# Kernel tuning notes

Measured on AMD Instinct MI355X. Metric: run time of the kernel, lower is better.

The kernel has to match this reference:

```python
import jax, jax.numpy as jnp
import numpy as np

# Module hyperparameters (init_kwargs): dim=128, res=128, idx=0, split_size=8, num_heads=8
B, RES, DIM, NH = 8, 128, 128, 8
HD = DIM // NH               # head_dim = 16
HSP, WSP = RES, 8            # idx=0 -> H_sp=res, W_sp=split_size
N = HSP * WSP                # tokens per window
SCALE = HD ** -0.5
L = RES * RES


def setup_inputs() -> dict:
    key = jax.random.key(0)
    k1, k2, k3 = jax.random.split(key, 3)
    return {
        "qkv": jax.random.normal(k1, (3, B, L, DIM), dtype=jnp.float32),
        "conv_w": jax.random.normal(k2, (DIM, 1, 3, 3), dtype=jnp.float32) * 0.1,
        "conv_b": jax.random.normal(k3, (DIM,), dtype=jnp.float32) * 0.1,
    }


def _im2cswin(x):
    # x: [B, L, C] -> windows as heads: [B*nW, NH, N, HD]
    x = jnp.transpose(x, (0, 2, 1)).reshape(B, DIM, RES, RES)
    x = x.reshape(B, DIM, RES // HSP, HSP, RES // WSP, WSP)
    x = jnp.transpose(x, (0, 2, 4, 3, 5, 1)).reshape(-1, N, DIM)
    x = x.reshape(-1, N, NH, HD)
    return jnp.transpose(x, (0, 2, 1, 3))


def reference(qkv, conv_w, conv_b):
    q, k, v = qkv[0], qkv[1], qkv[2]
    k = _im2cswin(k)                               # [W, NH, N, HD]
    v = _im2cswin(v)                               # [W, NH, N, HD]

    # q -> per-window image blocks [B*nW, C, H_sp, W_sp]
    qi = jnp.transpose(q, (0, 2, 1)).reshape(B, DIM, RES, RES)
    qi = qi.reshape(B, DIM, RES // HSP, HSP, RES // WSP, WSP)
    qi = jnp.transpose(qi, (0, 2, 4, 1, 3, 5)).reshape(-1, DIM, HSP, WSP)

    # depthwise 3x3 conv LePE
    lepe = jax.lax.conv_general_dilated(
        qi, conv_w, window_strides=(1, 1), padding='SAME',
        feature_group_count=DIM,
        dimension_numbers=('NCHW', 'OIHW', 'NCHW'))
    lepe = lepe + conv_b[None, :, None, None]
    lepe = jnp.transpose(lepe.reshape(-1, NH, HD, N), (0, 1, 3, 2))  # [W, NH, N, HD]
    qh = jnp.transpose(qi.reshape(-1, NH, HD, N), (0, 1, 3, 2))      # [W, NH, N, HD]

    # linear attention: softmax over scaled K^T V (d x d)
    att = jnp.einsum('wnid,wnie->wnde', k, v) * SCALE                # [W, NH, HD, HD]
    att = jax.nn.softmax(att, axis=-1)
    x = jnp.einsum('wnid,wnde->wnie', qh, att) + lepe                # [W, NH, N, HD]

    # windows -> image -> [B, L, C]
    x = jnp.transpose(x, (0, 2, 1, 3)).reshape(-1, N, DIM)
    x = x.reshape(B, RES // HSP, RES // WSP, HSP, WSP, DIM)
    x = jnp.transpose(x, (0, 1, 3, 2, 4, 5)).reshape(B, RES, RES, DIM)
    return x.reshape(B, L, DIM)
```

## Files before the change

### kernel.cpp

```cpp
#include <hip/hip_runtime.h>


static constexpr int BB   = 8;
static constexpr int RES  = 128;
static constexpr int DIM  = 128;
static constexpr int WSP  = 8;
static constexpr int L    = RES * RES;
static constexpr float SCALE = 0.25f;

#define GLD_LDS16(g, l)                                                        \
  __builtin_amdgcn_global_load_lds(                                            \
      (const __attribute__((address_space(1))) void*)(const void*)(g),         \
      (__attribute__((address_space(3))) void*)(l), 16, 0, 0)

__global__ __launch_bounds__(256, 2) void fused_lepe(
    const float* __restrict__ Qg, const float* __restrict__ Kg,
    const float* __restrict__ Vg, const float* __restrict__ cw,
    const float* __restrict__ cb, float* __restrict__ outp) {
  __shared__ float smem[16896];
  float* const A_sm = smem + 16384;

  const int b  = blockIdx.x;
  const int w  = b >> 2, g = b & 3;
  const int bi = w >> 4, wb = w & 15;
  const int t  = threadIdx.x;
  const int wave = t >> 6, lane = t & 63;
  const size_t win_base = (size_t)(bi * L + wb * WSP) * DIM;
  const int ch0 = g * 32;

  const int h1 = lane >> 5, dq = (lane >> 3) & 3, ep = lane & 7;
  float a00=0.f,a01=0.f,a10=0.f,a11=0.f,a20=0.f,a21=0.f,a30=0.f,a31=0.f;

  auto stageKV = [&](int tile, int buf) {
    for (int c = wave; c < 32; c += 4) {
      const int mat = c >> 4, rr = c & 15;
      const int r = tile * 16 + rr;
      const float* src = (mat ? Vg : Kg) + win_base +
                         (size_t)r * (RES * DIM) + (lane >> 3) * DIM + ch0 +
                         (lane & 7) * 4;
      float* dst = smem + mat * 8192 + buf * 4096 + rr * 256;
      GLD_LDS16(src, dst);
    }
  };

  stageKV(0, 0);
  __syncthreads();
  for (int tt = 0; tt < 8; ++tt) {
    const int cur = tt & 1;
    if (tt < 7) stageKV(tt + 1, cur ^ 1);
    const float* Kb = smem + cur * 4096;
    const float* Vb = smem + 8192 + cur * 4096;
    const int n0 = wave * 32;
#pragma unroll 4
    for (int n = n0; n < n0 + 32; ++n) {
      const float4 k4 =
          *reinterpret_cast<const float4*>(&Kb[n * 32 + h1 * 16 + dq * 4]);
      const float2 v2 =
          *reinterpret_cast<const float2*>(&Vb[n * 32 + h1 * 16 + ep * 2]);
      a00 += k4.x * v2.x; a01 += k4.x * v2.y;
      a10 += k4.y * v2.x; a11 += k4.y * v2.y;
      a20 += k4.z * v2.x; a21 += k4.z * v2.y;
      a30 += k4.w * v2.x; a31 += k4.w * v2.y;
    }
    __syncthreads();
  }

  auto stageQ = [&](int tile, int buf) {
    const int r0 = tile * 16;
    float* qb = smem + buf * 4608;
    for (int c = wave; c < 18; c += 4) {
      const int r = r0 - 1 + c;
      float* dst = qb + c * 256;
      if ((unsigned)r < 128u) {
        const float* src = Qg + win_base + (size_t)r * (RES * DIM) +
                           (lane >> 3) * DIM + ch0 + (lane & 7) * 4;
        GLD_LDS16(src, dst);
      } else {
        *reinterpret_cast<float4*>(dst + lane * 4) =
            make_float4(0.f, 0.f, 0.f, 0.f);
      }
    }
  };

  stageQ(0, 1);

  {
    float* sc = smem + wave * 512 + lane * 8;
    sc[0]=a00; sc[1]=a01; sc[2]=a10; sc[3]=a11;
    sc[4]=a20; sc[5]=a21; sc[6]=a30; sc[7]=a31;
  }
  __syncthreads();

  {
    const int r  = t >> 3;
    const int e2 = t & 7;
    const int h = r >> 4, d = r & 15;
    const int f = (h * 32 + (d >> 2) * 8 + e2) * 8 + (d & 3) * 2;
    float v0 = smem[f]     + smem[512 + f]     + smem[1024 + f]     + smem[1536 + f];
    float v1 = smem[f + 1] + smem[512 + f + 1] + smem[1024 + f + 1] + smem[1536 + f + 1];
    v0 *= SCALE; v1 *= SCALE;
    float m = fmaxf(v0, v1);
    m = fmaxf(m, __shfl_xor(m, 1));
    m = fmaxf(m, __shfl_xor(m, 2));
    m = fmaxf(m, __shfl_xor(m, 4));
    v0 = __expf(v0 - m); v1 = __expf(v1 - m);
    float ssum = v0 + v1;
    ssum += __shfl_xor(ssum, 1);
    ssum += __shfl_xor(ssum, 2);
    ssum += __shfl_xor(ssum, 4);
    const float rinv = 1.0f / ssum;
    A_sm[r * 16 + e2 * 2 + 0] = v0 * rinv;
    A_sm[r * 16 + e2 * 2 + 1] = v1 * rinv;
  }
  __syncthreads();

  const int cq   = t & 7;
  const int lr   = (t >> 3) & 15;
  const int half = t >> 7;
  const int hg = cq >> 2, e0 = (cq & 3) * 4;
  const int cg = ch0 + cq * 4;

  float4 Acol[16];
#pragma unroll
  for (int d = 0; d < 16; ++d)
    Acol[d] = *reinterpret_cast<const float4*>(&A_sm[(hg * 16 + d) * 16 + e0]);
  float4 wgt[9];
#pragma unroll
  for (int tap = 0; tap < 9; ++tap) {
    wgt[tap].x = cw[(cg + 0) * 9 + tap];
    wgt[tap].y = cw[(cg + 1) * 9 + tap];
    wgt[tap].z = cw[(cg + 2) * 9 + tap];
    wgt[tap].w = cw[(cg + 3) * 9 + tap];
  }
  const float4 bias = *reinterpret_cast<const float4*>(&cb[cg]);

#define ACC(qs, d)                                                             \
  o.x += (qs) * Acol[d].x; o.y += (qs) * Acol[d].y;                            \
  o.z += (qs) * Acol[d].z; o.w += (qs) * Acol[d].w;

  int buf = 1;
  for (int tile = 0; tile < 8; ++tile) {
    if (tile < 7) stageQ(tile + 1, buf ^ 1);
    const float* Qb = smem + buf * 4608;
    const int r0 = tile * 16;
    const int w0 = half * 4;

    float4 cL[3], cC[3], cR[3];
    auto ldcol = [&](int cidx, float4* dstv) {
#pragma unroll
      for (int dy = 0; dy < 3; ++dy)
        dstv[dy] = ((unsigned)cidx < 8u)
                       ? *reinterpret_cast<const float4*>(
                             &Qb[((lr + dy) * 8 + cidx) * 32 + cq * 4])
                       : make_float4(0.f, 0.f, 0.f, 0.f);
    };
    ldcol(w0 - 1, cL);
    ldcol(w0, cC);

#pragma unroll
    for (int k = 0; k < 4; ++k) {
      const int wl = w0 + k;
      ldcol(wl + 1, cR);
      float4 o = bias;
#pragma unroll
      for (int dy = 0; dy < 3; ++dy) {
        const int t0 = dy * 3;
        o.x += cL[dy].x * wgt[t0].x + cC[dy].x * wgt[t0+1].x + cR[dy].x * wgt[t0+2].x;
        o.y += cL[dy].y * wgt[t0].y + cC[dy].y * wgt[t0+1].y + cR[dy].y * wgt[t0+2].y;
        o.z += cL[dy].z * wgt[t0].z + cC[dy].z * wgt[t0+1].z + cR[dy].z * wgt[t0+2].z;
        o.w += cL[dy].w * wgt[t0].w + cC[dy].w * wgt[t0+1].w + cR[dy].w * wgt[t0+2].w;
      }
      const float* qr = &Qb[((lr + 1) * 8 + wl) * 32 + hg * 16];
      const float4 q0 = *reinterpret_cast<const float4*>(qr + 0);
      const float4 q1 = *reinterpret_cast<const float4*>(qr + 4);
      const float4 q2 = *reinterpret_cast<const float4*>(qr + 8);
      const float4 q3 = *reinterpret_cast<const float4*>(qr + 12);
      ACC(q0.x, 0)  ACC(q0.y, 1)  ACC(q0.z, 2)  ACC(q0.w, 3)
      ACC(q1.x, 4)  ACC(q1.y, 5)  ACC(q1.z, 6)  ACC(q1.w, 7)
      ACC(q2.x, 8)  ACC(q2.y, 9)  ACC(q2.z, 10) ACC(q2.w, 11)
      ACC(q3.x, 12) ACC(q3.y, 13) ACC(q3.z, 14) ACC(q3.w, 15)

      float* dst = outp + win_base + (size_t)(r0 + lr) * (RES * DIM) +
                   wl * DIM + cg;
      *reinterpret_cast<float4*>(dst) = o;

#pragma unroll
      for (int dy = 0; dy < 3; ++dy) { cL[dy] = cC[dy]; cC[dy] = cR[dy]; }
    }
    __syncthreads();
    buf ^= 1;
  }
#undef ACC
}

extern "C" void kernel_launch(void* const* d_in, const int* in_sizes, int n_in,
                              void* d_out, int out_size, void* d_ws,
                              size_t ws_size, hipStream_t stream) {
  const float* qkv = (const float*)d_in[0];
  const float* cw  = (const float*)d_in[1];
  const float* cb  = (const float*)d_in[2];
  const float* Qg = qkv;
  const float* Kg = qkv + (size_t)BB * L * DIM;
  const float* Vg = Kg + (size_t)BB * L * DIM;
  float* outp = (float*)d_out;

  fused_lepe<<<512, 256, 0, stream>>>(Qg, Kg, Vg, cw, cb, outp);
}
```

Baseline: 55.29 us.

## Triple-buffer KV staging, retile K^T V accumulation, swizzle Q LDS layout

The K^T V phase now stages 8-row tiles into a three-deep LDS ring, waiting with explicit vmcnt counts and raw barriers so loads run two tiles ahead. Each thread accumulates an 8x4 block from wider float4 reads, and partial sums are reduced across lane groups with shuffles instead of through LDS. The Q staging applies an XOR swizzle on the 16-byte column index, with matching reads in the conv and Q·A paths, to cut LDS bank conflicts. Shared memory drops, which may raise occupancy, but the hand-written waitcnt counts depend on the number of outstanding loads per thread and are fragile.

```diff
diff --git a/kernel.cpp b/kernel.cpp
--- a/kernel.cpp
+++ b/kernel.cpp
@@ -17,8 +17,9 @@
     const float* __restrict__ Qg, const float* __restrict__ Kg,
     const float* __restrict__ Vg, const float* __restrict__ cw,
     const float* __restrict__ cb, float* __restrict__ outp) {
-  __shared__ float smem[16896];
-  float* const A_sm = smem + 16384;
+  __shared__ float smem[12288];
+  float* const A_sm    = smem + 9216;
+  float* const scratch = smem + 10240;
 
   const int b  = blockIdx.x;
   const int w  = b >> 2, g = b & 3;
@@ -28,42 +29,65 @@
   const size_t win_base = (size_t)(bi * L + wb * WSP) * DIM;
   const int ch0 = g * 32;
 
-  const int h1 = lane >> 5, dq = (lane >> 3) & 3, ep = lane & 7;
-  float a00=0.f,a01=0.f,a10=0.f,a11=0.f,a20=0.f,a21=0.f,a30=0.f,a31=0.f;
+  const int combo = lane & 15;
+  const int split = lane >> 4;
+  const int h1 = combo >> 3, dgrp = (combo >> 2) & 1, eq = combo & 3;
+  const int koff = h1 * 16 + dgrp * 8;
+  const int voff = h1 * 16 + eq * 4;
+  const int n0 = (wave * 4 + split) * 4;
+
+  float4 acc[8];
+#pragma unroll
+  for (int i = 0; i < 8; ++i) acc[i] = make_float4(0.f, 0.f, 0.f, 0.f);
 
   auto stageKV = [&](int tile, int buf) {
-    for (int c = wave; c < 32; c += 4) {
-      const int mat = c >> 4, rr = c & 15;
-      const int r = tile * 16 + rr;
+    for (int c = wave; c < 16; c += 4) {
+      const int mat = c >> 3, rr = c & 7;
       const float* src = (mat ? Vg : Kg) + win_base +
-                         (size_t)r * (RES * DIM) + (lane >> 3) * DIM + ch0 +
-                         (lane & 7) * 4;
-      float* dst = smem + mat * 8192 + buf * 4096 + rr * 256;
+                         (size_t)(tile * 8 + rr) * (RES * DIM) +
+                         (lane >> 3) * DIM + ch0 + (lane & 7) * 4;
+      float* dst = smem + mat * 6144 + buf * 2048 + rr * 256;
       GLD_LDS16(src, dst);
     }
   };
 
   stageKV(0, 0);
+  stageKV(1, 1);
+  for (int tt = 0; tt < 16; ++tt) {
+    if (tt < 15) asm volatile("s_waitcnt vmcnt(4)" ::: "memory");
+    else         asm volatile("s_waitcnt vmcnt(0)" ::: "memory");
+    __builtin_amdgcn_s_barrier();
+    if (tt + 2 < 16) stageKV(tt + 2, (tt + 2) % 3);
+    const float* Kb = smem + (tt % 3) * 2048;
+    const float* Vb = smem + 6144 + (tt % 3) * 2048;
+#pragma unroll
+    for (int i = 0; i < 4; ++i) {
+      const int n = n0 + i;
+      const float4 k0 = *reinterpret_cast<const float4*>(&Kb[n * 32 + koff]);
+      const float4 k1 = *reinterpret_cast<const float4*>(&Kb[n * 32 + koff + 4]);
+      const float4 v  = *reinterpret_cast<const float4*>(&Vb[n * 32 + voff]);
+#define FMA4(a, s)                                                             \
+  a.x += (s) * v.x; a.y += (s) * v.y; a.z += (s) * v.z; a.w += (s) * v.w;
+      FMA4(acc[0], k0.x) FMA4(acc[1], k0.y) FMA4(acc[2], k0.z) FMA4(acc[3], k0.w)
+      FMA4(acc[4], k1.x) FMA4(acc[5], k1.y) FMA4(acc[6], k1.z) FMA4(acc[7], k1.w)
+#undef FMA4
+    }
+  }
+
+#pragma unroll
+  for (int i = 0; i < 8; ++i) {
+    acc[i].x += __shfl_xor(acc[i].x, 16); acc[i].y += __shfl_xor(acc[i].y, 16);
+    acc[i].z += __shfl_xor(acc[i].z, 16); acc[i].w += __shfl_xor(acc[i].w, 16);
+    acc[i].x += __shfl_xor(acc[i].x, 32); acc[i].y += __shfl_xor(acc[i].y, 32);
+    acc[i].z += __shfl_xor(acc[i].z, 32); acc[i].w += __shfl_xor(acc[i].w, 32);
+  }
+  if (lane < 16) {
+    float* sc = scratch + wave * 512 + combo * 32;
+#pragma unroll
+    for (int i = 0; i < 8; ++i)
+      *reinterpret_cast<float4*>(&sc[i * 4]) = acc[i];
+  }
   __syncthreads();
-  for (int tt = 0; tt < 8; ++tt) {
-    const int cur = tt & 1;
-    if (tt < 7) stageKV(tt + 1, cur ^ 1);
-    const float* Kb = smem + cur * 4096;
-    const float* Vb = smem + 8192 + cur * 4096;
-    const int n0 = wave * 32;
-#pragma unroll 4
-    for (int n = n0; n < n0 + 32; ++n) {
-      const float4 k4 =
-          *reinterpret_cast<const float4*>(&Kb[n * 32 + h1 * 16 + dq * 4]);
-      const float2 v2 =
-          *reinterpret_cast<const float2*>(&Vb[n * 32 + h1 * 16 + ep * 2]);
-      a00 += k4.x * v2.x; a01 += k4.x * v2.y;
-      a10 += k4.y * v2.x; a11 += k4.y * v2.y;
-      a20 += k4.z * v2.x; a21 += k4.z * v2.y;
-      a30 += k4.w * v2.x; a31 += k4.w * v2.y;
-    }
-    __syncthreads();
-  }
 
   auto stageQ = [&](int tile, int buf) {
     const int r0 = tile * 16;
@@ -73,7 +97,8 @@
       float* dst = qb + c * 256;
       if ((unsigned)r < 128u) {
         const float* src = Qg + win_base + (size_t)r * (RES * DIM) +
-                           (lane >> 3) * DIM + ch0 + (lane & 7) * 4;
+                           (lane >> 3) * DIM + ch0 +
+                           (((lane & 7) ^ (c & 7)) << 2);
         GLD_LDS16(src, dst);
       } else {
         *reinterpret_cast<float4*>(dst + lane * 4) =
@@ -81,36 +106,26 @@
       }
     }
   };
-
-  stageQ(0, 1);
+  stageQ(0, 0);
 
   {
-    float* sc = smem + wave * 512 + lane * 8;
-    sc[0]=a00; sc[1]=a01; sc[2]=a10; sc[3]=a11;
-    sc[4]=a20; sc[5]=a21; sc[6]=a30; sc[7]=a31;
-  }
-  __syncthreads();
-
-  {
-    const int r  = t >> 3;
-    const int e2 = t & 7;
-    const int h = r >> 4, d = r & 15;
-    const int f = (h * 32 + (d >> 2) * 8 + e2) * 8 + (d & 3) * 2;
-    float v0 = smem[f]     + smem[512 + f]     + smem[1024 + f]     + smem[1536 + f];
-    float v1 = smem[f + 1] + smem[512 + f + 1] + smem[1024 + f + 1] + smem[1536 + f + 1];
-    v0 *= SCALE; v1 *= SCALE;
+    const int r = t >> 3, e2 = t & 7;
+    const int cmb = (r >> 4) * 8 + ((r >> 3) & 1) * 4 + (e2 >> 1);
+    const float* s0 = scratch + cmb * 32 + (r & 7) * 4 + (e2 & 1) * 2;
+    float v0 = (s0[0] + s0[512] + s0[1024] + s0[1536]) * SCALE;
+    float v1 = (s0[1] + s0[513] + s0[1025] + s0[1537]) * SCALE;
     float m = fmaxf(v0, v1);
     m = fmaxf(m, __shfl_xor(m, 1));
     m = fmaxf(m, __shfl_xor(m, 2));
     m = fmaxf(m, __shfl_xor(m, 4));
     v0 = __expf(v0 - m); v1 = __expf(v1 - m);
-    float ssum = v0 + v1;
-    ssum += __shfl_xor(ssum, 1);
-    ssum += __shfl_xor(ssum, 2);
-    ssum += __shfl_xor(ssum, 4);
-    const float rinv = 1.0f / ssum;
-    A_sm[r * 16 + e2 * 2 + 0] = v0 * rinv;
-    A_sm[r * 16 + e2 * 2 + 1] = v1 * rinv;
+    float ss = v0 + v1;
+    ss += __shfl_xor(ss, 1);
+    ss += __shfl_xor(ss, 2);
+    ss += __shfl_xor(ss, 4);
+    const float ri = 1.0f / ss;
+    A_sm[r * 16 + e2 * 2 + 0] = v0 * ri;
+    A_sm[r * 16 + e2 * 2 + 1] = v1 * ri;
   }
   __syncthreads();
 
@@ -133,12 +148,13 @@
     wgt[tap].w = cw[(cg + 3) * 9 + tap];
   }
   const float4 bias = *reinterpret_cast<const float4*>(&cb[cg]);
+  const float4 zero4 = make_float4(0.f, 0.f, 0.f, 0.f);
 
 #define ACC(qs, d)                                                             \
   o.x += (qs) * Acol[d].x; o.y += (qs) * Acol[d].y;                            \
   o.z += (qs) * Acol[d].z; o.w += (qs) * Acol[d].w;
 
-  int buf = 1;
+  int buf = 0;
   for (int tile = 0; tile < 8; ++tile) {
     if (tile < 7) stageQ(tile + 1, buf ^ 1);
     const float* Qb = smem + buf * 4608;
@@ -146,13 +162,15 @@
     const int w0 = half * 4;
 
     float4 cL[3], cC[3], cR[3];
-    auto ldcol = [&](int cidx, float4* dstv) {
-#pragma unroll
-      for (int dy = 0; dy < 3; ++dy)
-        dstv[dy] = ((unsigned)cidx < 8u)
-                       ? *reinterpret_cast<const float4*>(
-                             &Qb[((lr + dy) * 8 + cidx) * 32 + cq * 4])
-                       : make_float4(0.f, 0.f, 0.f, 0.f);
+    auto ldcol = [&](int cidx, float4* dv) {
+#pragma unroll
+      for (int dy = 0; dy < 3; ++dy) {
+        const int br = lr + dy;
+        dv[dy] = ((unsigned)cidx < 8u)
+                     ? *reinterpret_cast<const float4*>(
+                           &Qb[(br * 8 + cidx) * 32 + ((cq ^ (br & 7)) << 2)])
+                     : zero4;
+      }
     };
     ldcol(w0 - 1, cL);
     ldcol(w0, cC);
@@ -170,16 +188,18 @@
         o.z += cL[dy].z * wgt[t0].z + cC[dy].z * wgt[t0+1].z + cR[dy].z * wgt[t0+2].z;
         o.w += cL[dy].w * wgt[t0].w + cC[dy].w * wgt[t0+1].w + cR[dy].w * wgt[t0+2].w;
       }
-      const float* qr = &Qb[((lr + 1) * 8 + wl) * 32 + hg * 16];
-      const float4 q0 = *reinterpret_cast<const float4*>(qr + 0);
-      const float4 q1 = *reinterpret_cast<const float4*>(qr + 4);
-      const float4 q2 = *reinterpret_cast<const float4*>(qr + 8);
-      const float4 q3 = *reinterpret_cast<const float4*>(qr + 12);
-      ACC(q0.x, 0)  ACC(q0.y, 1)  ACC(q0.z, 2)  ACC(q0.w, 3)
-      ACC(q1.x, 4)  ACC(q1.y, 5)  ACC(q1.z, 6)  ACC(q1.w, 7)
-      ACC(q2.x, 8)  ACC(q2.y, 9)  ACC(q2.z, 10) ACC(q2.w, 11)
-      ACC(q3.x, 12) ACC(q3.y, 13) ACC(q3.z, 14) ACC(q3.w, 15)
-
+      {
+        const int br1 = lr + 1, sw = br1 & 7;
+        const float* qb0 = &Qb[(br1 * 8 + wl) * 32];
+        const float4 q0 = *reinterpret_cast<const float4*>(qb0 + (((hg*4+0)^sw)<<2));
+        const float4 q1 = *reinterpret_cast<const float4*>(qb0 + (((hg*4+1)^sw)<<2));
+        const float4 q2 = *reinterpret_cast<const float4*>(qb0 + (((hg*4+2)^sw)<<2));
+        const float4 q3 = *reinterpret_cast<const float4*>(qb0 + (((hg*4+3)^sw)<<2));
+        ACC(q0.x, 0)  ACC(q0.y, 1)  ACC(q0.z, 2)  ACC(q0.w, 3)
+        ACC(q1.x, 4)  ACC(q1.y, 5)  ACC(q1.z, 6)  ACC(q1.w, 7)
+        ACC(q2.x, 8)  ACC(q2.y, 9)  ACC(q2.z, 10) ACC(q2.w, 11)
+        ACC(q3.x, 12) ACC(q3.y, 13) ACC(q3.z, 14) ACC(q3.w, 15)
+      }
       float* dst = outp + win_base + (size_t)(r0 + lr) * (RES * DIM) +
                    wl * DIM + cg;
       *reinterpret_cast<float4*>(dst) = o;
```

After: 67.51 us. 22.1% more time.
